# Kernel optimization log

Hardware: AMD Instinct MI355X
Metric: run time of the kernel (lower is better)

The kernel has to match this reference:

```python
import jax, jax.numpy as jnp
import numpy as np

N = 50000        # nodes
E = 800000       # directed edges (before self-loops)
F_IN = 128       # input node features
HID = 32         # hidden channels per head
HEADS = 4
NCLS = 8
EPS_BN = 1e-5
NEG_SLOPE = 0.2  # GATConv LeakyReLU default


def setup_inputs() -> dict:
    key = jax.random.key(0)
    ks = jax.random.split(key, 16)
    rn = lambda k, shape, s=0.1: jax.random.normal(k, shape, jnp.float32) * s
    inp = {}
    inp["x"] = jax.random.normal(ks[0], (N, F_IN), jnp.float32)
    inp["edge_index"] = jax.random.randint(ks[1], (2, E), 0, N, dtype=jnp.int32)
    # layer 0: F_IN -> HEADS*HID (concat)
    inp["W0"] = rn(ks[2], (F_IN, HEADS * HID))
    inp["as0"] = rn(ks[3], (HEADS, HID))
    inp["ad0"] = rn(ks[4], (HEADS, HID))
    inp["b0"] = jnp.zeros((HEADS * HID,), jnp.float32)
    inp["g0"] = jnp.ones((HEADS * HID,), jnp.float32)
    inp["bb0"] = jnp.zeros((HEADS * HID,), jnp.float32)
    inp["rm0"] = jnp.zeros((HEADS * HID,), jnp.float32)
    inp["rv0"] = jnp.ones((HEADS * HID,), jnp.float32)
    # layer 1: HEADS*HID -> HEADS*HID (concat)
    inp["W1"] = rn(ks[5], (HEADS * HID, HEADS * HID))
    inp["as1"] = rn(ks[6], (HEADS, HID))
    inp["ad1"] = rn(ks[7], (HEADS, HID))
    inp["b1"] = jnp.zeros((HEADS * HID,), jnp.float32)
    inp["g1"] = jnp.ones((HEADS * HID,), jnp.float32)
    inp["bb1"] = jnp.zeros((HEADS * HID,), jnp.float32)
    inp["rm1"] = jnp.zeros((HEADS * HID,), jnp.float32)
    inp["rv1"] = jnp.ones((HEADS * HID,), jnp.float32)
    # layer 2: HEADS*HID -> NCLS, heads=1, concat=False
    inp["W2"] = rn(ks[8], (HEADS * HID, NCLS))
    inp["as2"] = rn(ks[9], (1, NCLS))
    inp["ad2"] = rn(ks[10], (1, NCLS))
    inp["b2"] = jnp.zeros((NCLS,), jnp.float32)
    return inp


def gat_conv(x, src, dst, W, att_s, att_d, bias, H, C, concat):
    """PyG-style GATConv (eval mode, self-loops already appended to src/dst)."""
    n = x.shape[0]
    h = (x @ W).reshape(n, H, C)                       # [N,H,C]
    a_s = (h * att_s).sum(-1)                          # [N,H]
    a_d = (h * att_d).sum(-1)                          # [N,H]
    e = jax.nn.leaky_relu(a_s[src] + a_d[dst], NEG_SLOPE)  # [E,H]
    # numerically-stable segment softmax over incoming edges of each dst node
    m = jax.ops.segment_max(e, dst, num_segments=n)
    m = jnp.where(jnp.isfinite(m), m, 0.0)
    ex = jnp.exp(e - m[dst])
    den = jax.ops.segment_sum(ex, dst, num_segments=n)
    alpha = ex / (den[dst] + 1e-16)                    # [E,H]
    out = jax.ops.segment_sum(h[src] * alpha[:, :, None], dst, num_segments=n)  # [N,H,C]
    out = out.reshape(n, H * C) if concat else out.mean(axis=1)
    return out + bias


def bn_eval(x, g, b, rm, rv):
    return (x - rm) * jax.lax.rsqrt(rv + EPS_BN) * g + b


def reference(x, edge_index, W0, as0, ad0, b0, g0, bb0, rm0, rv0,
              W1, as1, ad1, b1, g1, bb1, rm1, rv1, W2, as2, ad2, b2):
    n = x.shape[0]
    loop = jnp.arange(n, dtype=edge_index.dtype)       # self-loops (PyG default)
    src = jnp.concatenate([edge_index[0], loop])
    dst = jnp.concatenate([edge_index[1], loop])
    h = gat_conv(x, src, dst, W0, as0, ad0, b0, HEADS, HID, True)
    h = jax.nn.elu(bn_eval(h, g0, bb0, rm0, rv0))
    h = gat_conv(h, src, dst, W1, as1, ad1, b1, HEADS, HID, True)
    h = jax.nn.elu(bn_eval(h, g1, bb1, rm1, rv1))
    h = gat_conv(h, src, dst, W2, as2, ad2, b2, 1, NCLS, False)
    return jax.nn.log_softmax(h, axis=1)
```

## Files before the change

### kernel.cpp

```cpp
#include <hip/hip_runtime.h>
#include <math.h>

#define N_NODES 50000
#define N_EDGES 800000
#define ET (N_EDGES + N_NODES)
#define FDIM 128
#define HEADS 4
#define HID 32
#define NCLS 8
#define NEG 0.2f
#define EPS_BN 1e-5f

#define BSH 8
#define NBUCK ((N_NODES + 255) >> BSH)
#define EPB 4096
#define PB ((ET + EPB - 1) / EPB)

typedef __attribute__((ext_vector_type(8))) short short8;
typedef __attribute__((ext_vector_type(4))) float f32x4;

__device__ __forceinline__ float lrelu(float e) { return e > 0.f ? e : NEG * e; }
__device__ __forceinline__ float bflo(unsigned u) { return __uint_as_float(u << 16); }
__device__ __forceinline__ float bfhi(unsigned u) { return __uint_as_float(u & 0xffff0000u); }
__device__ __forceinline__ unsigned f2bf(float f) {
    unsigned b = __float_as_uint(f);
    return (b + 0x7fffu + ((b >> 16) & 1u)) >> 16;
}


#define CAST_B 3125
#define PACK_B 64

__global__ __launch_bounds__(256) void prep_and_hist(
        const int* __restrict__ ei, int* __restrict__ bhist,
        const float* __restrict__ x, unsigned short* __restrict__ xb,
        const float* __restrict__ W0, unsigned short* __restrict__ W0p,
        const float* __restrict__ W1, unsigned short* __restrict__ W1p) {
    __shared__ unsigned h[NBUCK];
    int b = blockIdx.x, tid = threadIdx.x;
    if (b < PB) {
        int e0 = b * EPB;
        for (int i = tid; i < NBUCK; i += 256) h[i] = 0;
        __syncthreads();
        #pragma unroll
        for (int k = 0; k < EPB / 256; k++) {
            int e = e0 + k * 256 + tid;
            if (e < ET) {
                int d = (e < N_EDGES) ? ei[N_EDGES + e] : (e - N_EDGES);
                atomicAdd(&h[d >> BSH], 1u);
            }
        }
        __syncthreads();
        for (int i = tid; i < NBUCK; i += 256)
            if (h[i]) atomicAdd(&bhist[i], (int)h[i]);
    } else if (b < PB + CAST_B) {
        int i = (b - PB) * 256 + tid;
        const float4* p = (const float4*)x + (size_t)i * 2;
        float4 a = p[0], c = p[1];
        uint4 o;
        o.x = f2bf(a.x) | (f2bf(a.y) << 16);
        o.y = f2bf(a.z) | (f2bf(a.w) << 16);
        o.z = f2bf(c.x) | (f2bf(c.y) << 16);
        o.w = f2bf(c.z) | (f2bf(c.w) << 16);
        ((uint4*)xb)[i] = o;
    } else {
        int pb = b - PB - CAST_B;
        const float* W = (pb < PACK_B) ? W0 : W1;
        unsigned short* Wp = (pb < PACK_B) ? W0p : W1p;
        int o = (pb & (PACK_B - 1)) * 256 + tid;
        int j = o & 7, lane = (o >> 3) & 63, kc = (o >> 9) & 3, t = o >> 11;
        int k = kc * 32 + ((lane >> 4) << 3) + j;
        int n = t * 16 + (lane & 15);
        Wp[o] = (unsigned short)f2bf(W[k * 128 + n]);
    }
}

__global__ __launch_bounds__(256) void scan_buckets(const int* __restrict__ bhist,
                                                    int* __restrict__ boffs,
                                                    int* __restrict__ bcur,
                                                    int* __restrict__ offs) {
    __shared__ int s[256];
    int tid = threadIdx.x;
    int v = (tid < NBUCK) ? bhist[tid] : 0;
    s[tid] = v;
    __syncthreads();
    for (int off = 1; off < 256; off <<= 1) {
        int x = (tid >= off) ? s[tid - off] : 0;
        __syncthreads();
        s[tid] += x;
        __syncthreads();
    }
    int excl = s[tid] - v;
    if (tid < NBUCK) { boffs[tid] = excl; bcur[tid] = excl; }
    if (tid == 0) { boffs[NBUCK] = ET; offs[N_NODES] = ET; }
}

__global__ __launch_bounds__(256) void partition_pairs(const int* __restrict__ ei,
                                                       int* __restrict__ bcur,
                                                       int2* __restrict__ pairs) {
    __shared__ unsigned hist[NBUCK];
    __shared__ unsigned base[NBUCK];
    int tid = threadIdx.x;
    int e0 = blockIdx.x * EPB;
    for (int i = tid; i < NBUCK; i += 256) hist[i] = 0;
    __syncthreads();
    #pragma unroll
    for (int k = 0; k < EPB / 256; k++) {
        int e = e0 + k * 256 + tid;
        if (e < ET) {
            int d = (e < N_EDGES) ? ei[N_EDGES + e] : (e - N_EDGES);
            atomicAdd(&hist[d >> BSH], 1u);
        }
    }
    __syncthreads();
    for (int i = tid; i < NBUCK; i += 256) {
        unsigned h = hist[i];
        base[i] = h ? (unsigned)atomicAdd(&bcur[i], (int)h) : 0u;
        hist[i] = 0;
    }
    __syncthreads();
    #pragma unroll
    for (int k = 0; k < EPB / 256; k++) {
        int e = e0 + k * 256 + tid;
        if (e < ET) {
            int s, d;
            if (e < N_EDGES) { s = ei[e]; d = ei[N_EDGES + e]; }
            else             { s = d = e - N_EDGES; }
            int b = d >> BSH;
            unsigned lpos = atomicAdd(&hist[b], 1u);
            pairs[base[b] + lpos] = make_int2(s, d);
        }
    }
}

__global__ __launch_bounds__(256) void group_bucket(const int2* __restrict__ pairs,
                                                    const int* __restrict__ boffs,
                                                    int* __restrict__ offs,
                                                    int* __restrict__ ssrc) {
    __shared__ int cnt[256];
    __shared__ int pfx[256];
    int b = blockIdx.x, tid = threadIdx.x;
    int n0 = b << BSH;
    int base = boffs[b], end = boffs[b + 1];
    cnt[tid] = 0;
    __syncthreads();
    for (int i = base + tid; i < end; i += 256)
        atomicAdd(&cnt[pairs[i].y & 255], 1);
    __syncthreads();
    int v = cnt[tid];
    pfx[tid] = v;
    __syncthreads();
    for (int off = 1; off < 256; off <<= 1) {
        int x = (tid >= off) ? pfx[tid - off] : 0;
        __syncthreads();
        pfx[tid] += x;
        __syncthreads();
    }
    int excl = pfx[tid] - v;
    if (n0 + tid < N_NODES) offs[n0 + tid] = base + excl;
    cnt[tid] = excl;
    __syncthreads();
    for (int i = base + tid; i < end; i += 256) {
        int2 p = pairs[i];
        int pos = atomicAdd(&cnt[p.y & 255], 1);
        ssrc[base + pos] = p.x;
    }
}


__global__ __launch_bounds__(256) void gemm_attn(
        const unsigned short* __restrict__ Ab, const unsigned short* __restrict__ Wp,
        const float* __restrict__ att_s, const float* __restrict__ att_d,
        unsigned short* __restrict__ Hb, float* __restrict__ asn, float* __restrict__ adn,
        int M) {
    __shared__ float tiles[64 * 132];
    int tid = threadIdx.x;
    int wv = tid >> 6, lane = tid & 63;
    int base = blockIdx.x * 64;
    int mrow = base + wv * 16 + (lane & 15);
    if (mrow >= M) mrow = M - 1;
    int koff = (lane >> 4) * 8;

    f32x4 acc[8];
    #pragma unroll
    for (int t = 0; t < 8; t++) acc[t] = (f32x4){0.f, 0.f, 0.f, 0.f};

    #pragma unroll
    for (int kc = 0; kc < 4; kc++) {
        short8 a = *(const short8*)(Ab + (size_t)mrow * 128 + kc * 32 + koff);
        #pragma unroll
        for (int t = 0; t < 8; t++) {
            short8 b = *(const short8*)(Wp + (((t * 4 + kc) * 64 + lane) << 3));
            acc[t] = __builtin_amdgcn_mfma_f32_16x16x32_bf16(a, b, acc[t], 0, 0, 0);
        }
    }

    int rbase = wv * 16 + (lane >> 4) * 4;
    int col = lane & 15;
    #pragma unroll
    for (int t = 0; t < 8; t++)
        #pragma unroll
        for (int r = 0; r < 4; r++)
            tiles[(rbase + r) * 132 + t * 16 + col] = acc[t][r];
    __syncthreads();

    #pragma unroll
    for (int it = 0; it < 4; it++) {
        int u = tid + it * 256;
        int rl = u >> 4, cg = u & 15;
        int row = base + rl;
        if (row < M) {
            const float* p = tiles + rl * 132 + cg * 8;
            float4 v0 = *(const float4*)(p);
            float4 v1 = *(const float4*)(p + 4);
            uint4 o;
            o.x = f2bf(v0.x) | (f2bf(v0.y) << 16);
            o.y = f2bf(v0.z) | (f2bf(v0.w) << 16);
            o.z = f2bf(v1.x) | (f2bf(v1.y) << 16);
            o.w = f2bf(v1.z) | (f2bf(v1.w) << 16);
            *(uint4*)(Hb + (size_t)row * 128 + cg * 8) = o;
        }
    }

    {
        int rl = tid >> 2, hd = tid & 3;
        int row = base + rl;
        if (row < M) {
            const float* hrow = tiles + rl * 132 + hd * 32;
            const float* as = att_s + hd * 32;
            const float* ad = att_d + hd * 32;
            float ps = 0.f, pd = 0.f;
            #pragma unroll
            for (int i = 0; i < 8; i++) {
                float4 hv = *(const float4*)(hrow + i * 4);
                float4 sv = *(const float4*)(as + i * 4);
                float4 dv = *(const float4*)(ad + i * 4);
                ps += hv.x * sv.x + hv.y * sv.y + hv.z * sv.z + hv.w * sv.w;
                pd += hv.x * dv.x + hv.y * dv.y + hv.z * dv.z + hv.w * dv.w;
            }
            asn[row * 4 + hd] = ps;
            adn[row * 4 + hd] = pd;
        }
    }
}


__global__ __launch_bounds__(256) void aggregate(
        const unsigned short* __restrict__ hb, const float* __restrict__ asn,
        const float* __restrict__ adn, const int* __restrict__ offs,
        const int* __restrict__ ssrc, const float* __restrict__ bias,
        const float* __restrict__ gamma, const float* __restrict__ beta,
        const float* __restrict__ rmean, const float* __restrict__ rvar,
        unsigned short* __restrict__ outb) {
    __shared__ int2 sPair[4][4][72];
    int wv = threadIdx.x >> 6;
    int node = blockIdx.x * 4 + wv;
    if (node >= N_NODES) return;
    int lane = threadIdx.x & 63;
    int half = lane >> 5;
    int cl = lane & 31;
    int hd = lane >> 4;
    int beg = offs[node], deg = offs[node + 1] - beg;
    float4 ad4 = *(const float4*)(adn + node * 4);

    float4 den4 = make_float4(0.f, 0.f, 0.f, 0.f);
    float a0 = 0.f, a1 = 0.f, a2 = 0.f, a3 = 0.f;
    const char* hbase = (const char*)hb + cl * 8;
    int hsel = (cl >> 3);
    const int2* pp = &sPair[wv][hsel][0];

    auto phaseC = [&](int cnt) {
        int bound = (cnt + 15) & ~15;
        for (int i = 0; i < bound; i += 16) {
            int2 p0 = pp[i + 0 + half],  p1 = pp[i + 2 + half];
            int2 p2 = pp[i + 4 + half],  p3 = pp[i + 6 + half];
            int2 p4 = pp[i + 8 + half],  p5 = pp[i + 10 + half];
            int2 p6 = pp[i + 12 + half], p7 = pp[i + 14 + half];
            uint2 u0 = *(const uint2*)(hbase + (unsigned)p0.x);
            uint2 u1 = *(const uint2*)(hbase + (unsigned)p1.x);
            uint2 u2 = *(const uint2*)(hbase + (unsigned)p2.x);
            uint2 u3 = *(const uint2*)(hbase + (unsigned)p3.x);
            uint2 u4 = *(const uint2*)(hbase + (unsigned)p4.x);
            uint2 u5 = *(const uint2*)(hbase + (unsigned)p5.x);
            uint2 u6 = *(const uint2*)(hbase + (unsigned)p6.x);
            uint2 u7 = *(const uint2*)(hbase + (unsigned)p7.x);
            float w0 = __int_as_float(p0.y), w1 = __int_as_float(p1.y);
            float w2 = __int_as_float(p2.y), w3 = __int_as_float(p3.y);
            float w4 = __int_as_float(p4.y), w5 = __int_as_float(p5.y);
            float w6 = __int_as_float(p6.y), w7 = __int_as_float(p7.y);
            a0 += w0 * bflo(u0.x); a1 += w0 * bfhi(u0.x); a2 += w0 * bflo(u0.y); a3 += w0 * bfhi(u0.y);
            a0 += w1 * bflo(u1.x); a1 += w1 * bfhi(u1.x); a2 += w1 * bflo(u1.y); a3 += w1 * bfhi(u1.y);
            a0 += w2 * bflo(u2.x); a1 += w2 * bfhi(u2.x); a2 += w2 * bflo(u2.y); a3 += w2 * bfhi(u2.y);
            a0 += w3 * bflo(u3.x); a1 += w3 * bfhi(u3.x); a2 += w3 * bflo(u3.y); a3 += w3 * bfhi(u3.y);
            a0 += w4 * bflo(u4.x); a1 += w4 * bfhi(u4.x); a2 += w4 * bflo(u4.y); a3 += w4 * bfhi(u4.y);
            a0 += w5 * bflo(u5.x); a1 += w5 * bfhi(u5.x); a2 += w5 * bflo(u5.y); a3 += w5 * bfhi(u5.y);
            a0 += w6 * bflo(u6.x); a1 += w6 * bfhi(u6.x); a2 += w6 * bflo(u6.y); a3 += w6 * bfhi(u6.y);
            a0 += w7 * bflo(u7.x); a1 += w7 * bfhi(u7.x); a2 += w7 * bflo(u7.y); a3 += w7 * bfhi(u7.y);
        }
    };

    for (int base0 = 0; base0 < deg; base0 += 64) {
        int j = base0 + lane;
        int soff = 0;
        float4 w4v = make_float4(0.f, 0.f, 0.f, 0.f);
        if (j < deg) {
            int s = ssrc[beg + j];
            soff = s << 8;
            float4 a = *(const float4*)(asn + s * 4);
            w4v.x = __expf(lrelu(a.x + ad4.x));
            w4v.y = __expf(lrelu(a.y + ad4.y));
            w4v.z = __expf(lrelu(a.z + ad4.z));
            w4v.w = __expf(lrelu(a.w + ad4.w));
            den4.x += w4v.x; den4.y += w4v.y; den4.z += w4v.z; den4.w += w4v.w;
        }
        sPair[wv][0][lane] = make_int2(soff, __float_as_int(w4v.x));
        sPair[wv][1][lane] = make_int2(soff, __float_as_int(w4v.y));
        sPair[wv][2][lane] = make_int2(soff, __float_as_int(w4v.z));
        sPair[wv][3][lane] = make_int2(soff, __float_as_int(w4v.w));
        int cnt = deg - base0; if (cnt > 64) cnt = 64;
        phaseC(cnt);
    }
    (void)hd;

    a0 += __shfl_xor(a0, 32); a1 += __shfl_xor(a1, 32);
    a2 += __shfl_xor(a2, 32); a3 += __shfl_xor(a3, 32);
    #pragma unroll
    for (int off = 32; off; off >>= 1) {
        den4.x += __shfl_xor(den4.x, off);
        den4.y += __shfl_xor(den4.y, off);
        den4.z += __shfl_xor(den4.z, off);
        den4.w += __shfl_xor(den4.w, off);
    }
    if (half == 0) {
        float den = (hsel & 2) ? ((hsel & 1) ? den4.w : den4.z)
                               : ((hsel & 1) ? den4.y : den4.x);
        float inv = 1.f / (den + 1e-16f);
        int c0 = cl * 4;
        float4 bi = *(const float4*)(bias + c0);
        float4 gm = *(const float4*)(gamma + c0);
        float4 bt = *(const float4*)(beta + c0);
        float4 rm = *(const float4*)(rmean + c0);
        float4 rv = *(const float4*)(rvar + c0);
        float o0 = a0 * inv + bi.x, o1 = a1 * inv + bi.y;
        float o2 = a2 * inv + bi.z, o3 = a3 * inv + bi.w;
        o0 = (o0 - rm.x) * rsqrtf(rv.x + EPS_BN) * gm.x + bt.x;
        o1 = (o1 - rm.y) * rsqrtf(rv.y + EPS_BN) * gm.y + bt.y;
        o2 = (o2 - rm.z) * rsqrtf(rv.z + EPS_BN) * gm.z + bt.z;
        o3 = (o3 - rm.w) * rsqrtf(rv.w + EPS_BN) * gm.w + bt.w;
        o0 = (o0 > 0.f) ? o0 : expm1f(o0);
        o1 = (o1 > 0.f) ? o1 : expm1f(o1);
        o2 = (o2 > 0.f) ? o2 : expm1f(o2);
        o3 = (o3 > 0.f) ? o3 : expm1f(o3);
        uint2 ob;
        ob.x = f2bf(o0) | (f2bf(o1) << 16);
        ob.y = f2bf(o2) | (f2bf(o3) << 16);
        *(uint2*)(outb + (size_t)node * 128 + c0) = ob;
    }
}


__global__ __launch_bounds__(256) void gemm2_fused(
        const unsigned short* __restrict__ xb, const float* __restrict__ W2,
        const float* __restrict__ as2, const float* __restrict__ ad2,
        float* __restrict__ h2, float* __restrict__ asn, float* __restrict__ adn) {
    __shared__ float sW[128 * 8];
    __shared__ float sas[8], sad[8];
    int tid = threadIdx.x;
    for (int i = tid; i < 1024; i += 256) sW[i] = W2[i];
    if (tid < 8) { sas[tid] = as2[tid]; sad[tid] = ad2[tid]; }
    __syncthreads();
    int node = blockIdx.x * 256 + tid;
    if (node >= N_NODES) return;
    const uint4* xr = (const uint4*)(xb + (size_t)node * 128);
    float acc[8];
    #pragma unroll
    for (int c = 0; c < 8; c++) acc[c] = 0.f;
    for (int k8 = 0; k8 < 16; k8++) {
        uint4 u = xr[k8];
        float f[8] = { bflo(u.x), bfhi(u.x), bflo(u.y), bfhi(u.y),
                       bflo(u.z), bfhi(u.z), bflo(u.w), bfhi(u.w) };
        int kb = k8 * 8;
        #pragma unroll
        for (int q = 0; q < 8; q++)
            #pragma unroll
            for (int c = 0; c < 8; c++)
                acc[c] += f[q] * sW[(kb + q) * 8 + c];
    }
    float ps = 0.f, pd = 0.f;
    #pragma unroll
    for (int c = 0; c < 8; c++) {
        h2[(size_t)node * 8 + c] = acc[c];
        ps += acc[c] * sas[c];
        pd += acc[c] * sad[c];
    }
    asn[node] = ps;
    adn[node] = pd;
}


__global__ __launch_bounds__(256) void aggregate2(
        const float* __restrict__ h2, const float* __restrict__ asn,
        const float* __restrict__ adn, const int* __restrict__ offs,
        const int* __restrict__ ssrc, const float* __restrict__ b2,
        float* __restrict__ out) {
    __shared__ int2 sPair[4][64];
    int wv = threadIdx.x >> 6;
    int node = blockIdx.x * 4 + wv;
    if (node >= N_NODES) return;
    int lane = threadIdx.x & 63;
    int g = lane >> 3, c = lane & 7;
    int beg = offs[node], end = offs[node + 1];
    int deg = end - beg;
    float adv = adn[node];

    float den = 0.f, acc = 0.f;
    auto phaseC = [&](int cnt) {
        int nIt = (cnt + 15) >> 4;
        const int2* pp = &sPair[wv][0];
        for (int i = 0; i < nIt; i++) {
            int e = i * 16 + g;
            int2 p0 = pp[e];
            int2 p1 = pp[e + 8];
            acc += __int_as_float(p0.y) * h2[(((unsigned)p0.x) << 3) + c];
            acc += __int_as_float(p1.y) * h2[(((unsigned)p1.x) << 3) + c];
        }
    };

    for (int base = 0; base < deg; base += 64) {
        int j = base + lane;
        int s = 0; float w = 0.f;
        if (j < deg) {
            s = ssrc[beg + j];
            w = __expf(lrelu(asn[s] + adv));
            den += w;
        }
        sPair[wv][lane] = make_int2(s, __float_as_int(w));
        int cnt = deg - base; if (cnt > 64) cnt = 64;
        phaseC(cnt);
    }

    acc += __shfl_xor(acc, 8); acc += __shfl_xor(acc, 16); acc += __shfl_xor(acc, 32);
    #pragma unroll
    for (int off = 32; off; off >>= 1) den += __shfl_xor(den, off);

    float o = acc / (den + 1e-16f) + b2[c];
    float mx = o;
    mx = fmaxf(mx, __shfl_xor(mx, 1));
    mx = fmaxf(mx, __shfl_xor(mx, 2));
    mx = fmaxf(mx, __shfl_xor(mx, 4));
    float ex = __expf(o - mx);
    float sm = ex;
    sm += __shfl_xor(sm, 1); sm += __shfl_xor(sm, 2); sm += __shfl_xor(sm, 4);
    if (g == 0) out[(size_t)node * 8 + c] = o - mx - logf(sm);
}


extern "C" void kernel_launch(void* const* d_in, const int* in_sizes, int n_in,
                              void* d_out, int out_size, void* d_ws, size_t ws_size,
                              hipStream_t stream) {
    const float* x   = (const float*)d_in[0];
    const int*   ei  = (const int*)d_in[1];
    const float* W0  = (const float*)d_in[2];
    const float* as0 = (const float*)d_in[3];
    const float* ad0 = (const float*)d_in[4];
    const float* b0  = (const float*)d_in[5];
    const float* g0  = (const float*)d_in[6];
    const float* bb0 = (const float*)d_in[7];
    const float* rm0 = (const float*)d_in[8];
    const float* rv0 = (const float*)d_in[9];
    const float* W1  = (const float*)d_in[10];
    const float* as1 = (const float*)d_in[11];
    const float* ad1 = (const float*)d_in[12];
    const float* b1  = (const float*)d_in[13];
    const float* g1  = (const float*)d_in[14];
    const float* bb1 = (const float*)d_in[15];
    const float* rm1 = (const float*)d_in[16];
    const float* rv1 = (const float*)d_in[17];
    const float* W2  = (const float*)d_in[18];
    const float* as2 = (const float*)d_in[19];
    const float* ad2 = (const float*)d_in[20];
    const float* b2  = (const float*)d_in[21];
    float* out = (float*)d_out;

    char* w = (char*)d_ws;
    size_t off = 0;
    auto carve = [&](size_t bytes) {
        void* p = w + off;
        off += (bytes + 255) & ~(size_t)255;
        return p;
    };
    unsigned short* xb   = (unsigned short*)carve((size_t)N_NODES * 128 * 2);
    unsigned short* Hb   = (unsigned short*)carve((size_t)N_NODES * 128 * 2);
    unsigned short* Xb   = (unsigned short*)carve((size_t)N_NODES * 128 * 2);
    unsigned short* W0p  = (unsigned short*)carve(16384 * 2);
    unsigned short* W1p  = (unsigned short*)carve(16384 * 2);
    int*   offs   = (int*)carve((size_t)(N_NODES + 1) * 4);
    int*   bhist  = (int*)carve((size_t)NBUCK * 4);
    int*   boffs  = (int*)carve((size_t)(NBUCK + 1) * 4);
    int*   bcur   = (int*)carve((size_t)NBUCK * 4);
    int*   ssrc   = (int*)carve((size_t)ET * 4);
    int2*  pairs  = (int2*)carve((size_t)ET * 8);
    float* asn    = (float*)carve((size_t)N_NODES * 4 * 4);
    float* adn    = (float*)carve((size_t)N_NODES * 4 * 4);
    float* h2     = (float*)carve((size_t)N_NODES * 8 * 4);
    float* as2n   = (float*)carve((size_t)N_NODES * 4);
    float* ad2n   = (float*)carve((size_t)N_NODES * 4);
    (void)ws_size; (void)in_sizes; (void)n_in; (void)out_size;

    const int NB = (N_NODES + 255) / 256;
    const int GB = (N_NODES + 63) / 64;

    hipMemsetAsync(bhist, 0, (size_t)NBUCK * 4, stream);
    prep_and_hist<<<PB + CAST_B + 2 * PACK_B, 256, 0, stream>>>(ei, bhist, x, xb,
                                                                W0, W0p, W1, W1p);
    scan_buckets<<<1, 256, 0, stream>>>(bhist, boffs, bcur, offs);
    partition_pairs<<<PB, 256, 0, stream>>>(ei, bcur, pairs);
    group_bucket<<<NBUCK, 256, 0, stream>>>(pairs, boffs, offs, ssrc);

    gemm_attn<<<GB, 256, 0, stream>>>(xb, W0p, as0, ad0, Hb, asn, adn, N_NODES);
    aggregate<<<(N_NODES + 3) / 4, 256, 0, stream>>>(Hb, asn, adn, offs, ssrc,
                                                     b0, g0, bb0, rm0, rv0, Xb);
    gemm_attn<<<GB, 256, 0, stream>>>(Xb, W1p, as1, ad1, Hb, asn, adn, N_NODES);
    aggregate<<<(N_NODES + 3) / 4, 256, 0, stream>>>(Hb, asn, adn, offs, ssrc,
                                                     b1, g1, bb1, rm1, rv1, Xb);
    gemm2_fused<<<NB, 256, 0, stream>>>(Xb, W2, as2, ad2, h2, as2n, ad2n);
    aggregate2<<<(N_NODES + 3) / 4, 256, 0, stream>>>(h2, as2n, ad2n, offs, ssrc, b2, out);
}
```

Measured before the change: 295.6 us.

## Fuse all GAT stages into one cooperative persistent kernel with grid syncs

Turns every stage (CSR build, the two GEMM+attention passes, aggregations, final layer) into device functions, and runs them inside one cooperative kernel that loops over work units and separates stages with grid.sync. This removes about ten kernel launches and the memset. The global atomic bucket histogram becomes per-block histograms that the scan reduces, so no zero-initialisation is needed. It keeps a multi-kernel fallback for when a cooperative launch is unavailable, but trades launch gaps for grid-barrier cost and fewer resident blocks per stage.

```diff
diff --git a/kernel.cpp b/kernel.cpp
--- a/kernel.cpp
+++ b/kernel.cpp
@@ -1,13 +1,12 @@
 #include <hip/hip_runtime.h>
+#include <hip/hip_cooperative_groups.h>
 #include <math.h>
+
+namespace cg = cooperative_groups;
 
 #define N_NODES 50000
 #define N_EDGES 800000
 #define ET (N_EDGES + N_NODES)
-#define FDIM 128
-#define HEADS 4
-#define HID 32
-#define NCLS 8
 #define NEG 0.2f
 #define EPS_BN 1e-5f
 
@@ -15,6 +14,12 @@
 #define NBUCK ((N_NODES + 255) >> BSH)
 #define EPB 4096
 #define PB ((ET + EPB - 1) / EPB)
+#define CAST_B 3125
+#define PACK_B 64
+#define GB ((N_NODES + 63) / 64)
+#define AGG_U 12500
+#define G2B ((N_NODES + 255) / 256)
+#define PREP_U (PB + CAST_B + 2 * PACK_B)
 
 typedef __attribute__((ext_vector_type(8))) short short8;
 typedef __attribute__((ext_vector_type(4))) float f32x4;
@@ -27,21 +32,31 @@
     return (b + 0x7fffu + ((b >> 16) & 1u)) >> 16;
 }
 
-
-#define CAST_B 3125
-#define PACK_B 64
-
-__global__ __launch_bounds__(256) void prep_and_hist(
-        const int* __restrict__ ei, int* __restrict__ bhist,
+struct GatParams {
+    const int* ei;
+    const float* x;
+    const float *W0, *as0, *ad0, *b0, *g0, *bb0, *rm0, *rv0;
+    const float *W1, *as1, *ad1, *b1, *g1, *bb1, *rm1, *rv1;
+    const float *W2, *as2, *ad2, *b2;
+    float* out;
+    unsigned short *xb, *Hb, *Xb, *W0p, *W1p;
+    int *offs, *boffs, *bcur, *ssrc, *hists;
+    int2* pairs;
+    float *asn, *adn, *h2;
+};
+
+
+__device__ __forceinline__ void prep_unit(char* smem, int u, int tid,
+        const int* __restrict__ ei, int* __restrict__ hists,
         const float* __restrict__ x, unsigned short* __restrict__ xb,
         const float* __restrict__ W0, unsigned short* __restrict__ W0p,
         const float* __restrict__ W1, unsigned short* __restrict__ W1p) {
-    __shared__ unsigned h[NBUCK];
-    int b = blockIdx.x, tid = threadIdx.x;
-    if (b < PB) {
-        int e0 = b * EPB;
+    if (u < PB) {
+        unsigned* h = (unsigned*)smem;
+        __syncthreads();
         for (int i = tid; i < NBUCK; i += 256) h[i] = 0;
         __syncthreads();
+        int e0 = u * EPB;
         #pragma unroll
         for (int k = 0; k < EPB / 256; k++) {
             int e = e0 + k * 256 + tid;
@@ -52,11 +67,11 @@
         }
         __syncthreads();
         for (int i = tid; i < NBUCK; i += 256)
-            if (h[i]) atomicAdd(&bhist[i], (int)h[i]);
-    } else if (b < PB + CAST_B) {
-        int i = (b - PB) * 256 + tid;
-        const float4* p = (const float4*)x + (size_t)i * 2;
-        float4 a = p[0], c = p[1];
+            hists[u * NBUCK + i] = (int)h[i];
+    } else if (u < PB + CAST_B) {
+        int i = (u - PB) * 256 + tid;
+        const float4* px = (const float4*)x + (size_t)i * 2;
+        float4 a = px[0], c = px[1];
         uint4 o;
         o.x = f2bf(a.x) | (f2bf(a.y) << 16);
         o.y = f2bf(a.z) | (f2bf(a.w) << 16);
@@ -64,7 +79,7 @@
         o.w = f2bf(c.z) | (f2bf(c.w) << 16);
         ((uint4*)xb)[i] = o;
     } else {
-        int pb = b - PB - CAST_B;
+        int pb = u - PB - CAST_B;
         const float* W = (pb < PACK_B) ? W0 : W1;
         unsigned short* Wp = (pb < PACK_B) ? W0p : W1p;
         int o = (pb & (PACK_B - 1)) * 256 + tid;
@@ -75,13 +90,16 @@
     }
 }
 
-__global__ __launch_bounds__(256) void scan_buckets(const int* __restrict__ bhist,
-                                                    int* __restrict__ boffs,
-                                                    int* __restrict__ bcur,
-                                                    int* __restrict__ offs) {
-    __shared__ int s[256];
-    int tid = threadIdx.x;
-    int v = (tid < NBUCK) ? bhist[tid] : 0;
+__device__ __forceinline__ void scan_unit(char* smem, int tid,
+        const int* __restrict__ hists, int* __restrict__ boffs,
+        int* __restrict__ bcur, int* __restrict__ offs) {
+    int* s = (int*)smem;
+    int v = 0;
+    if (tid < NBUCK) {
+        const int* hp = hists + tid;
+        #pragma unroll 8
+        for (int uu = 0; uu < PB; uu++) v += hp[uu * NBUCK];
+    }
     s[tid] = v;
     __syncthreads();
     for (int off = 1; off < 256; off <<= 1) {
@@ -93,17 +111,17 @@
     int excl = s[tid] - v;
     if (tid < NBUCK) { boffs[tid] = excl; bcur[tid] = excl; }
     if (tid == 0) { boffs[NBUCK] = ET; offs[N_NODES] = ET; }
-}
-
-__global__ __launch_bounds__(256) void partition_pairs(const int* __restrict__ ei,
-                                                       int* __restrict__ bcur,
-                                                       int2* __restrict__ pairs) {
-    __shared__ unsigned hist[NBUCK];
-    __shared__ unsigned base[NBUCK];
-    int tid = threadIdx.x;
-    int e0 = blockIdx.x * EPB;
+    __syncthreads();
+}
+
+__device__ __forceinline__ void partition_unit(char* smem, int u, int tid,
+        const int* __restrict__ ei, int* __restrict__ bcur, int2* __restrict__ pairs) {
+    unsigned* hist = (unsigned*)smem;
+    unsigned* base = hist + NBUCK;
+    __syncthreads();
     for (int i = tid; i < NBUCK; i += 256) hist[i] = 0;
     __syncthreads();
+    int e0 = u * EPB;
     #pragma unroll
     for (int k = 0; k < EPB / 256; k++) {
         int e = e0 + k * 256 + tid;
@@ -114,8 +132,8 @@
     }
     __syncthreads();
     for (int i = tid; i < NBUCK; i += 256) {
-        unsigned h = hist[i];
-        base[i] = h ? (unsigned)atomicAdd(&bcur[i], (int)h) : 0u;
+        unsigned hh = hist[i];
+        base[i] = hh ? (unsigned)atomicAdd(&bcur[i], (int)hh) : 0u;
         hist[i] = 0;
     }
     __syncthreads();
@@ -133,15 +151,14 @@
     }
 }
 
-__global__ __launch_bounds__(256) void group_bucket(const int2* __restrict__ pairs,
-                                                    const int* __restrict__ boffs,
-                                                    int* __restrict__ offs,
-                                                    int* __restrict__ ssrc) {
-    __shared__ int cnt[256];
-    __shared__ int pfx[256];
-    int b = blockIdx.x, tid = threadIdx.x;
-    int n0 = b << BSH;
-    int base = boffs[b], end = boffs[b + 1];
+__device__ __forceinline__ void group_unit(char* smem, int u, int tid,
+        const int2* __restrict__ pairs, const int* __restrict__ boffs,
+        int* __restrict__ offs, int* __restrict__ ssrc) {
+    int* cnt = (int*)smem;
+    int* pfx = cnt + 256;
+    __syncthreads();
+    int n0 = u << BSH;
+    int base = boffs[u], end = boffs[u + 1];
     cnt[tid] = 0;
     __syncthreads();
     for (int i = base + tid; i < end; i += 256)
@@ -161,224 +178,211 @@
     cnt[tid] = excl;
     __syncthreads();
     for (int i = base + tid; i < end; i += 256) {
-        int2 p = pairs[i];
-        int pos = atomicAdd(&cnt[p.y & 255], 1);
-        ssrc[base + pos] = p.x;
-    }
-}
-
-
-__global__ __launch_bounds__(256) void gemm_attn(
+        int2 pr = pairs[i];
+        int pos = atomicAdd(&cnt[pr.y & 255], 1);
+        ssrc[base + pos] = pr.x;
+    }
+}
+
+__device__ __forceinline__ void gemm_phase(char* smem, int blk, int nblk,
         const unsigned short* __restrict__ Ab, const unsigned short* __restrict__ Wp,
         const float* __restrict__ att_s, const float* __restrict__ att_d,
-        unsigned short* __restrict__ Hb, float* __restrict__ asn, float* __restrict__ adn,
-        int M) {
-    __shared__ float tiles[64 * 132];
+        unsigned short* __restrict__ Hb, float* __restrict__ asn, float* __restrict__ adn) {
+    float* tiles = (float*)smem;
     int tid = threadIdx.x;
     int wv = tid >> 6, lane = tid & 63;
-    int base = blockIdx.x * 64;
-    int mrow = base + wv * 16 + (lane & 15);
-    if (mrow >= M) mrow = M - 1;
-    int koff = (lane >> 4) * 8;
-
-    f32x4 acc[8];
-    #pragma unroll
-    for (int t = 0; t < 8; t++) acc[t] = (f32x4){0.f, 0.f, 0.f, 0.f};
-
-    #pragma unroll
-    for (int kc = 0; kc < 4; kc++) {
-        short8 a = *(const short8*)(Ab + (size_t)mrow * 128 + kc * 32 + koff);
+    for (int u = blk; u < GB; u += nblk) {
+        int base = u * 64;
+        int mrow = base + wv * 16 + (lane & 15);
+        if (mrow >= N_NODES) mrow = N_NODES - 1;
+        int koff = (lane >> 4) * 8;
+
+        f32x4 acc[8];
         #pragma unroll
-        for (int t = 0; t < 8; t++) {
-            short8 b = *(const short8*)(Wp + (((t * 4 + kc) * 64 + lane) << 3));
-            acc[t] = __builtin_amdgcn_mfma_f32_16x16x32_bf16(a, b, acc[t], 0, 0, 0);
-        }
-    }
-
-    int rbase = wv * 16 + (lane >> 4) * 4;
-    int col = lane & 15;
-    #pragma unroll
-    for (int t = 0; t < 8; t++)
+        for (int t = 0; t < 8; t++) acc[t] = (f32x4){0.f, 0.f, 0.f, 0.f};
         #pragma unroll
-        for (int r = 0; r < 4; r++)
-            tiles[(rbase + r) * 132 + t * 16 + col] = acc[t][r];
-    __syncthreads();
-
-    #pragma unroll
-    for (int it = 0; it < 4; it++) {
-        int u = tid + it * 256;
-        int rl = u >> 4, cg = u & 15;
-        int row = base + rl;
-        if (row < M) {
-            const float* p = tiles + rl * 132 + cg * 8;
-            float4 v0 = *(const float4*)(p);
-            float4 v1 = *(const float4*)(p + 4);
-            uint4 o;
-            o.x = f2bf(v0.x) | (f2bf(v0.y) << 16);
-            o.y = f2bf(v0.z) | (f2bf(v0.w) << 16);
-            o.z = f2bf(v1.x) | (f2bf(v1.y) << 16);
-            o.w = f2bf(v1.z) | (f2bf(v1.w) << 16);
-            *(uint4*)(Hb + (size_t)row * 128 + cg * 8) = o;
-        }
-    }
-
-    {
-        int rl = tid >> 2, hd = tid & 3;
-        int row = base + rl;
-        if (row < M) {
-            const float* hrow = tiles + rl * 132 + hd * 32;
-            const float* as = att_s + hd * 32;
-            const float* ad = att_d + hd * 32;
-            float ps = 0.f, pd = 0.f;
+        for (int kc = 0; kc < 4; kc++) {
+            short8 a = *(const short8*)(Ab + (size_t)mrow * 128 + kc * 32 + koff);
             #pragma unroll
-            for (int i = 0; i < 8; i++) {
-                float4 hv = *(const float4*)(hrow + i * 4);
-                float4 sv = *(const float4*)(as + i * 4);
-                float4 dv = *(const float4*)(ad + i * 4);
-                ps += hv.x * sv.x + hv.y * sv.y + hv.z * sv.z + hv.w * sv.w;
-                pd += hv.x * dv.x + hv.y * dv.y + hv.z * dv.z + hv.w * dv.w;
+            for (int t = 0; t < 8; t++) {
+                short8 b = *(const short8*)(Wp + (((t * 4 + kc) * 64 + lane) << 3));
+                acc[t] = __builtin_amdgcn_mfma_f32_16x16x32_bf16(a, b, acc[t], 0, 0, 0);
             }
-            asn[row * 4 + hd] = ps;
-            adn[row * 4 + hd] = pd;
-        }
-    }
-}
-
-
-__global__ __launch_bounds__(256) void aggregate(
+        }
+        __syncthreads();
+        int rbase = wv * 16 + (lane >> 4) * 4;
+        int col = lane & 15;
+        #pragma unroll
+        for (int t = 0; t < 8; t++)
+            #pragma unroll
+            for (int r = 0; r < 4; r++)
+                tiles[(rbase + r) * 132 + t * 16 + col] = acc[t][r];
+        __syncthreads();
+
+        #pragma unroll
+        for (int it = 0; it < 4; it++) {
+            int uu = tid + it * 256;
+            int rl = uu >> 4, cg4 = uu & 15;
+            int row = base + rl;
+            if (row < N_NODES) {
+                const float* pt = tiles + rl * 132 + cg4 * 8;
+                float4 v0 = *(const float4*)(pt);
+                float4 v1 = *(const float4*)(pt + 4);
+                uint4 o;
+                o.x = f2bf(v0.x) | (f2bf(v0.y) << 16);
+                o.y = f2bf(v0.z) | (f2bf(v0.w) << 16);
+                o.z = f2bf(v1.x) | (f2bf(v1.y) << 16);
+                o.w = f2bf(v1.z) | (f2bf(v1.w) << 16);
+                *(uint4*)(Hb + (size_t)row * 128 + cg4 * 8) = o;
+            }
+        }
+        {
+            int rl = tid >> 2, hd = tid & 3;
+            int row = base + rl;
+            if (row < N_NODES) {
+                const float* hrow = tiles + rl * 132 + hd * 32;
+                const float* as = att_s + hd * 32;
+                const float* ad = att_d + hd * 32;
+                float ps = 0.f, pd = 0.f;
+                #pragma unroll
+                for (int i = 0; i < 8; i++) {
+                    float4 hv = *(const float4*)(hrow + i * 4);
+                    float4 sv = *(const float4*)(as + i * 4);
+                    float4 dv = *(const float4*)(ad + i * 4);
+                    ps += hv.x * sv.x + hv.y * sv.y + hv.z * sv.z + hv.w * sv.w;
+                    pd += hv.x * dv.x + hv.y * dv.y + hv.z * dv.z + hv.w * dv.w;
+                }
+                asn[row * 4 + hd] = ps;
+                adn[row * 4 + hd] = pd;
+            }
+        }
+        __syncthreads();
+    }
+}
+
+__device__ __forceinline__ void aggregate_phase(char* smem, int blk, int nblk,
         const unsigned short* __restrict__ hb, const float* __restrict__ asn,
         const float* __restrict__ adn, const int* __restrict__ offs,
         const int* __restrict__ ssrc, const float* __restrict__ bias,
         const float* __restrict__ gamma, const float* __restrict__ beta,
         const float* __restrict__ rmean, const float* __restrict__ rvar,
         unsigned short* __restrict__ outb) {
-    __shared__ int2 sPair[4][4][72];
-    int wv = threadIdx.x >> 6;
-    int node = blockIdx.x * 4 + wv;
-    if (node >= N_NODES) return;
-    int lane = threadIdx.x & 63;
-    int half = lane >> 5;
-    int cl = lane & 31;
-    int hd = lane >> 4;
-    int beg = offs[node], deg = offs[node + 1] - beg;
-    float4 ad4 = *(const float4*)(adn + node * 4);
-
-    float4 den4 = make_float4(0.f, 0.f, 0.f, 0.f);
-    float a0 = 0.f, a1 = 0.f, a2 = 0.f, a3 = 0.f;
+    int2* sP = (int2*)smem;
+    int tid = threadIdx.x;
+    int wv = tid >> 6, lane = tid & 63;
+    int half = lane >> 5, cl = lane & 31, hsel = cl >> 3;
     const char* hbase = (const char*)hb + cl * 8;
-    int hsel = (cl >> 3);
-    const int2* pp = &sPair[wv][hsel][0];
-
-    auto phaseC = [&](int cnt) {
-        int bound = (cnt + 15) & ~15;
-        for (int i = 0; i < bound; i += 16) {
-            int2 p0 = pp[i + 0 + half],  p1 = pp[i + 2 + half];
-            int2 p2 = pp[i + 4 + half],  p3 = pp[i + 6 + half];
-            int2 p4 = pp[i + 8 + half],  p5 = pp[i + 10 + half];
-            int2 p6 = pp[i + 12 + half], p7 = pp[i + 14 + half];
-            uint2 u0 = *(const uint2*)(hbase + (unsigned)p0.x);
-            uint2 u1 = *(const uint2*)(hbase + (unsigned)p1.x);
-            uint2 u2 = *(const uint2*)(hbase + (unsigned)p2.x);
-            uint2 u3 = *(const uint2*)(hbase + (unsigned)p3.x);
-            uint2 u4 = *(const uint2*)(hbase + (unsigned)p4.x);
-            uint2 u5 = *(const uint2*)(hbase + (unsigned)p5.x);
-            uint2 u6 = *(const uint2*)(hbase + (unsigned)p6.x);
-            uint2 u7 = *(const uint2*)(hbase + (unsigned)p7.x);
-            float w0 = __int_as_float(p0.y), w1 = __int_as_float(p1.y);
-            float w2 = __int_as_float(p2.y), w3 = __int_as_float(p3.y);
-            float w4 = __int_as_float(p4.y), w5 = __int_as_float(p5.y);
-            float w6 = __int_as_float(p6.y), w7 = __int_as_float(p7.y);
-            a0 += w0 * bflo(u0.x); a1 += w0 * bfhi(u0.x); a2 += w0 * bflo(u0.y); a3 += w0 * bfhi(u0.y);
-            a0 += w1 * bflo(u1.x); a1 += w1 * bfhi(u1.x); a2 += w1 * bflo(u1.y); a3 += w1 * bfhi(u1.y);
-            a0 += w2 * bflo(u2.x); a1 += w2 * bfhi(u2.x); a2 += w2 * bflo(u2.y); a3 += w2 * bfhi(u2.y);
-            a0 += w3 * bflo(u3.x); a1 += w3 * bfhi(u3.x); a2 += w3 * bflo(u3.y); a3 += w3 * bfhi(u3.y);
-            a0 += w4 * bflo(u4.x); a1 += w4 * bfhi(u4.x); a2 += w4 * bflo(u4.y); a3 += w4 * bfhi(u4.y);
-            a0 += w5 * bflo(u5.x); a1 += w5 * bfhi(u5.x); a2 += w5 * bflo(u5.y); a3 += w5 * bfhi(u5.y);
-            a0 += w6 * bflo(u6.x); a1 += w6 * bfhi(u6.x); a2 += w6 * bflo(u6.y); a3 += w6 * bfhi(u6.y);
-            a0 += w7 * bflo(u7.x); a1 += w7 * bfhi(u7.x); a2 += w7 * bflo(u7.y); a3 += w7 * bfhi(u7.y);
-        }
-    };
-
-    for (int base0 = 0; base0 < deg; base0 += 64) {
-        int j = base0 + lane;
-        int soff = 0;
-        float4 w4v = make_float4(0.f, 0.f, 0.f, 0.f);
-        if (j < deg) {
-            int s = ssrc[beg + j];
-            soff = s << 8;
-            float4 a = *(const float4*)(asn + s * 4);
-            w4v.x = __expf(lrelu(a.x + ad4.x));
-            w4v.y = __expf(lrelu(a.y + ad4.y));
-            w4v.z = __expf(lrelu(a.z + ad4.z));
-            w4v.w = __expf(lrelu(a.w + ad4.w));
-            den4.x += w4v.x; den4.y += w4v.y; den4.z += w4v.z; den4.w += w4v.w;
-        }
-        sPair[wv][0][lane] = make_int2(soff, __float_as_int(w4v.x));
-        sPair[wv][1][lane] = make_int2(soff, __float_as_int(w4v.y));
-        sPair[wv][2][lane] = make_int2(soff, __float_as_int(w4v.z));
-        sPair[wv][3][lane] = make_int2(soff, __float_as_int(w4v.w));
-        int cnt = deg - base0; if (cnt > 64) cnt = 64;
-        phaseC(cnt);
-    }
-    (void)hd;
-
-    a0 += __shfl_xor(a0, 32); a1 += __shfl_xor(a1, 32);
-    a2 += __shfl_xor(a2, 32); a3 += __shfl_xor(a3, 32);
-    #pragma unroll
-    for (int off = 32; off; off >>= 1) {
-        den4.x += __shfl_xor(den4.x, off);
-        den4.y += __shfl_xor(den4.y, off);
-        den4.z += __shfl_xor(den4.z, off);
-        den4.w += __shfl_xor(den4.w, off);
-    }
-    if (half == 0) {
-        float den = (hsel & 2) ? ((hsel & 1) ? den4.w : den4.z)
-                               : ((hsel & 1) ? den4.y : den4.x);
-        float inv = 1.f / (den + 1e-16f);
-        int c0 = cl * 4;
-        float4 bi = *(const float4*)(bias + c0);
-        float4 gm = *(const float4*)(gamma + c0);
-        float4 bt = *(const float4*)(beta + c0);
-        float4 rm = *(const float4*)(rmean + c0);
-        float4 rv = *(const float4*)(rvar + c0);
-        float o0 = a0 * inv + bi.x, o1 = a1 * inv + bi.y;
-        float o2 = a2 * inv + bi.z, o3 = a3 * inv + bi.w;
-        o0 = (o0 - rm.x) * rsqrtf(rv.x + EPS_BN) * gm.x + bt.x;
-        o1 = (o1 - rm.y) * rsqrtf(rv.y + EPS_BN) * gm.y + bt.y;
-        o2 = (o2 - rm.z) * rsqrtf(rv.z + EPS_BN) * gm.z + bt.z;
-        o3 = (o3 - rm.w) * rsqrtf(rv.w + EPS_BN) * gm.w + bt.w;
-        o0 = (o0 > 0.f) ? o0 : expm1f(o0);
-        o1 = (o1 > 0.f) ? o1 : expm1f(o1);
-        o2 = (o2 > 0.f) ? o2 : expm1f(o2);
-        o3 = (o3 > 0.f) ? o3 : expm1f(o3);
-        uint2 ob;
-        ob.x = f2bf(o0) | (f2bf(o1) << 16);
-        ob.y = f2bf(o2) | (f2bf(o3) << 16);
-        *(uint2*)(outb + (size_t)node * 128 + c0) = ob;
-    }
-}
-
-
-__global__ __launch_bounds__(256) void gemm2_fused(
+    int2* st0 = sP + (wv * 4 + 0) * 72;
+    int2* st1 = sP + (wv * 4 + 1) * 72;
+    int2* st2 = sP + (wv * 4 + 2) * 72;
+    int2* st3 = sP + (wv * 4 + 3) * 72;
+    const int2* pp = sP + (wv * 4 + hsel) * 72;
+
+    for (int u = blk; u < AGG_U; u += nblk) {
+        int node = u * 4 + wv;
+        int beg = offs[node], deg = offs[node + 1] - beg;
+        float4 ad4 = *(const float4*)(adn + node * 4);
+        float a0 = 0.f, a1 = 0.f, a2 = 0.f, a3 = 0.f, denl = 0.f;
+
+        for (int base0 = 0; base0 < deg; base0 += 64) {
+            int j = base0 + lane;
+            int soff = 0;
+            float4 w4v = make_float4(0.f, 0.f, 0.f, 0.f);
+            if (j < deg) {
+                int s = ssrc[beg + j];
+                soff = s << 8;
+                float4 a = *(const float4*)(asn + s * 4);
+                w4v.x = __expf(lrelu(a.x + ad4.x));
+                w4v.y = __expf(lrelu(a.y + ad4.y));
+                w4v.z = __expf(lrelu(a.z + ad4.z));
+                w4v.w = __expf(lrelu(a.w + ad4.w));
+            }
+            st0[lane] = make_int2(soff, __float_as_int(w4v.x));
+            st1[lane] = make_int2(soff, __float_as_int(w4v.y));
+            st2[lane] = make_int2(soff, __float_as_int(w4v.z));
+            st3[lane] = make_int2(soff, __float_as_int(w4v.w));
+            int cnt = deg - base0; if (cnt > 64) cnt = 64;
+            int bound = (cnt + 15) & ~15;
+            for (int i = 0; i < bound; i += 16) {
+                int2 p0 = pp[i + 0 + half],  p1 = pp[i + 2 + half];
+                int2 p2 = pp[i + 4 + half],  p3 = pp[i + 6 + half];
+                int2 p4 = pp[i + 8 + half],  p5 = pp[i + 10 + half];
+                int2 p6 = pp[i + 12 + half], p7 = pp[i + 14 + half];
+                uint2 u0 = *(const uint2*)(hbase + (unsigned)p0.x);
+                uint2 u1 = *(const uint2*)(hbase + (unsigned)p1.x);
+                uint2 u2 = *(const uint2*)(hbase + (unsigned)p2.x);
+                uint2 u3 = *(const uint2*)(hbase + (unsigned)p3.x);
+                uint2 u4 = *(const uint2*)(hbase + (unsigned)p4.x);
+                uint2 u5 = *(const uint2*)(hbase + (unsigned)p5.x);
+                uint2 u6 = *(const uint2*)(hbase + (unsigned)p6.x);
+                uint2 u7 = *(const uint2*)(hbase + (unsigned)p7.x);
+                float w0 = __int_as_float(p0.y), w1 = __int_as_float(p1.y);
+                float w2 = __int_as_float(p2.y), w3 = __int_as_float(p3.y);
+                float w4 = __int_as_float(p4.y), w5 = __int_as_float(p5.y);
+                float w6 = __int_as_float(p6.y), w7 = __int_as_float(p7.y);
+                denl += w0 + w1 + w2 + w3 + w4 + w5 + w6 + w7;
+                a0 += w0 * bflo(u0.x); a1 += w0 * bfhi(u0.x); a2 += w0 * bflo(u0.y); a3 += w0 * bfhi(u0.y);
+                a0 += w1 * bflo(u1.x); a1 += w1 * bfhi(u1.x); a2 += w1 * bflo(u1.y); a3 += w1 * bfhi(u1.y);
+                a0 += w2 * bflo(u2.x); a1 += w2 * bfhi(u2.x); a2 += w2 * bflo(u2.y); a3 += w2 * bfhi(u2.y);
+                a0 += w3 * bflo(u3.x); a1 += w3 * bfhi(u3.x); a2 += w3 * bflo(u3.y); a3 += w3 * bfhi(u3.y);
+                a0 += w4 * bflo(u4.x); a1 += w4 * bfhi(u4.x); a2 += w4 * bflo(u4.y); a3 += w4 * bfhi(u4.y);
+                a0 += w5 * bflo(u5.x); a1 += w5 * bfhi(u5.x); a2 += w5 * bflo(u5.y); a3 += w5 * bfhi(u5.y);
+                a0 += w6 * bflo(u6.x); a1 += w6 * bfhi(u6.x); a2 += w6 * bflo(u6.y); a3 += w6 * bfhi(u6.y);
+                a0 += w7 * bflo(u7.x); a1 += w7 * bfhi(u7.x); a2 += w7 * bflo(u7.y); a3 += w7 * bfhi(u7.y);
+            }
+        }
+        a0 += __shfl_xor(a0, 32); a1 += __shfl_xor(a1, 32);
+        a2 += __shfl_xor(a2, 32); a3 += __shfl_xor(a3, 32);
+        denl += __shfl_xor(denl, 32);
+        if (half == 0) {
+            float inv = 1.f / (denl + 1e-16f);
+            int c0 = cl * 4;
+            float4 bi = *(const float4*)(bias + c0);
+            float4 gm = *(const float4*)(gamma + c0);
+            float4 bt = *(const float4*)(beta + c0);
+            float4 rm = *(const float4*)(rmean + c0);
+            float4 rv = *(const float4*)(rvar + c0);
+            float o0 = a0 * inv + bi.x, o1 = a1 * inv + bi.y;
+            float o2 = a2 * inv + bi.z, o3 = a3 * inv + bi.w;
+            o0 = (o0 - rm.x) * rsqrtf(rv.x + EPS_BN) * gm.x + bt.x;
+            o1 = (o1 - rm.y) * rsqrtf(rv.y + EPS_BN) * gm.y + bt.y;
+            o2 = (o2 - rm.z) * rsqrtf(rv.z + EPS_BN) * gm.z + bt.z;
+            o3 = (o3 - rm.w) * rsqrtf(rv.w + EPS_BN) * gm.w + bt.w;
+            o0 = (o0 > 0.f) ? o0 : expm1f(o0);
+            o1 = (o1 > 0.f) ? o1 : expm1f(o1);
+            o2 = (o2 > 0.f) ? o2 : expm1f(o2);
+            o3 = (o3 > 0.f) ? o3 : expm1f(o3);
+            uint2 ob;
+            ob.x = f2bf(o0) | (f2bf(o1) << 16);
+            ob.y = f2bf(o2) | (f2bf(o3) << 16);
+            *(uint2*)(outb + (size_t)node * 128 + c0) = ob;
+        }
+    }
+}
+
+__device__ __forceinline__ void gemm2_unit(char* smem, int u, int tid,
         const unsigned short* __restrict__ xb, const float* __restrict__ W2,
         const float* __restrict__ as2, const float* __restrict__ ad2,
-        float* __restrict__ h2, float* __restrict__ asn, float* __restrict__ adn) {
-    __shared__ float sW[128 * 8];
-    __shared__ float sas[8], sad[8];
-    int tid = threadIdx.x;
-    for (int i = tid; i < 1024; i += 256) sW[i] = W2[i];
-    if (tid < 8) { sas[tid] = as2[tid]; sad[tid] = ad2[tid]; }
-    __syncthreads();
-    int node = blockIdx.x * 256 + tid;
+        float* __restrict__ h2, float* __restrict__ asn, float* __restrict__ adn,
+        bool loadW) {
+    float* sW = (float*)smem;
+    float* sas = sW + 1024;
+    float* sad = sas + 8;
+    if (loadW) {
+        for (int i = tid; i < 1024; i += 256) sW[i] = W2[i];
+        if (tid < 8) { sas[tid] = as2[tid]; sad[tid] = ad2[tid]; }
+        __syncthreads();
+    }
+    int node = u * 256 + tid;
     if (node >= N_NODES) return;
     const uint4* xr = (const uint4*)(xb + (size_t)node * 128);
     float acc[8];
     #pragma unroll
     for (int c = 0; c < 8; c++) acc[c] = 0.f;
     for (int k8 = 0; k8 < 16; k8++) {
-        uint4 u = xr[k8];
-        float f[8] = { bflo(u.x), bfhi(u.x), bflo(u.y), bfhi(u.y),
-                       bflo(u.z), bfhi(u.z), bflo(u.w), bfhi(u.w) };
+        uint4 uu = xr[k8];
+        float f[8] = { bflo(uu.x), bfhi(uu.x), bflo(uu.y), bfhi(uu.y),
+                       bflo(uu.z), bfhi(uu.z), bflo(uu.w), bfhi(uu.w) };
         int kb = k8 * 8;
         #pragma unroll
         for (int q = 0; q < 8; q++)
@@ -397,35 +401,20 @@
     adn[node] = pd;
 }
 
-
-__global__ __launch_bounds__(256) void aggregate2(
+__device__ __forceinline__ void agg2_unit(char* smem, int u, int tid,
         const float* __restrict__ h2, const float* __restrict__ asn,
         const float* __restrict__ adn, const int* __restrict__ offs,
         const int* __restrict__ ssrc, const float* __restrict__ b2,
         float* __restrict__ out) {
-    __shared__ int2 sPair[4][64];
-    int wv = threadIdx.x >> 6;
-    int node = blockIdx.x * 4 + wv;
-    if (node >= N_NODES) return;
-    int lane = threadIdx.x & 63;
+    int2* sP = (int2*)smem;
+    int wv = tid >> 6, lane = tid & 63;
     int g = lane >> 3, c = lane & 7;
+    int node = u * 4 + wv;
     int beg = offs[node], end = offs[node + 1];
     int deg = end - beg;
     float adv = adn[node];
-
     float den = 0.f, acc = 0.f;
-    auto phaseC = [&](int cnt) {
-        int nIt = (cnt + 15) >> 4;
-        const int2* pp = &sPair[wv][0];
-        for (int i = 0; i < nIt; i++) {
-            int e = i * 16 + g;
-            int2 p0 = pp[e];
-            int2 p1 = pp[e + 8];
-            acc += __int_as_float(p0.y) * h2[(((unsigned)p0.x) << 3) + c];
-            acc += __int_as_float(p1.y) * h2[(((unsigned)p1.x) << 3) + c];
-        }
-    };
-
+    int2* ws = sP + wv * 64;
     for (int base = 0; base < deg; base += 64) {
         int j = base + lane;
         int s = 0; float w = 0.f;
@@ -434,15 +423,20 @@
             w = __expf(lrelu(asn[s] + adv));
             den += w;
         }
-        sPair[wv][lane] = make_int2(s, __float_as_int(w));
+        ws[lane] = make_int2(s, __float_as_int(w));
         int cnt = deg - base; if (cnt > 64) cnt = 64;
-        phaseC(cnt);
-    }
-
+        int nIt = (cnt + 15) >> 4;
+        for (int i = 0; i < nIt; i++) {
+            int e = i * 16 + g;
+            int2 p0 = ws[e];
+            int2 p1 = ws[e + 8];
+            acc += __int_as_float(p0.y) * h2[(((unsigned)p0.x) << 3) + c];
+            acc += __int_as_float(p1.y) * h2[(((unsigned)p1.x) << 3) + c];
+        }
+    }
     acc += __shfl_xor(acc, 8); acc += __shfl_xor(acc, 16); acc += __shfl_xor(acc, 32);
     #pragma unroll
     for (int off = 32; off; off >>= 1) den += __shfl_xor(den, off);
-
     float o = acc / (den + 1e-16f) + b2[c];
     float mx = o;
     mx = fmaxf(mx, __shfl_xor(mx, 1));
@@ -455,32 +449,125 @@
 }
 
 
+__global__ __launch_bounds__(256, 3) void gat_mega(GatParams p) {
+    cg::grid_group grid = cg::this_grid();
+    __shared__ __align__(16) char smem[64 * 132 * 4];
+    const int blk = blockIdx.x, nblk = gridDim.x, tid = threadIdx.x;
+
+    for (int u = blk; u < PREP_U; u += nblk)
+        prep_unit(smem, u, tid, p.ei, p.hists, p.x, p.xb, p.W0, p.W0p, p.W1, p.W1p);
+    grid.sync();
+
+    if (blk == 0) scan_unit(smem, tid, p.hists, p.boffs, p.bcur, p.offs);
+    gemm_phase(smem, blk, nblk, p.xb, p.W0p, p.as0, p.ad0, p.Hb, p.asn, p.adn);
+    grid.sync();
+
+    for (int u = blk; u < PB; u += nblk)
+        partition_unit(smem, u, tid, p.ei, p.bcur, p.pairs);
+    grid.sync();
+
+    for (int u = blk; u < NBUCK; u += nblk)
+        group_unit(smem, u, tid, p.pairs, p.boffs, p.offs, p.ssrc);
+    grid.sync();
+
+    aggregate_phase(smem, blk, nblk, p.Hb, p.asn, p.adn, p.offs, p.ssrc,
+                    p.b0, p.g0, p.bb0, p.rm0, p.rv0, p.Xb);
+    grid.sync();
+
+    gemm_phase(smem, blk, nblk, p.Xb, p.W1p, p.as1, p.ad1, p.Hb, p.asn, p.adn);
+    grid.sync();
+
+    aggregate_phase(smem, blk, nblk, p.Hb, p.asn, p.adn, p.offs, p.ssrc,
+                    p.b1, p.g1, p.bb1, p.rm1, p.rv1, p.Xb);
+    grid.sync();
+
+    {
+        float* sW = (float*)smem;
+        float* sas = sW + 1024;
+        float* sad = sas + 8;
+        __syncthreads();
+        for (int i = tid; i < 1024; i += 256) sW[i] = p.W2[i];
+        if (tid < 8) { sas[tid] = p.as2[tid]; sad[tid] = p.ad2[tid]; }
+        __syncthreads();
+        for (int u = blk; u < G2B; u += nblk)
+            gemm2_unit(smem, u, tid, p.Xb, p.W2, p.as2, p.ad2, p.h2, p.asn, p.adn, false);
+    }
+    grid.sync();
+
+    for (int u = blk; u < AGG_U; u += nblk) {
+        __syncthreads();
+        agg2_unit(smem, u, tid, p.h2, p.asn, p.adn, p.offs, p.ssrc, p.b2, p.out);
+    }
+}
+
+
+__global__ __launch_bounds__(256) void k_prep(GatParams p) {
+    __shared__ __align__(16) char smem[1024];
+    prep_unit(smem, blockIdx.x, threadIdx.x, p.ei, p.hists, p.x, p.xb,
+              p.W0, p.W0p, p.W1, p.W1p);
+}
+__global__ __launch_bounds__(256) void k_scan(GatParams p) {
+    __shared__ __align__(16) char smem[1024];
+    scan_unit(smem, threadIdx.x, p.hists, p.boffs, p.bcur, p.offs);
+}
+__global__ __launch_bounds__(256) void k_partition(GatParams p) {
+    __shared__ __align__(16) char smem[2048];
+    partition_unit(smem, blockIdx.x, threadIdx.x, p.ei, p.bcur, p.pairs);
+}
+__global__ __launch_bounds__(256) void k_group(GatParams p) {
+    __shared__ __align__(16) char smem[2048];
+    group_unit(smem, blockIdx.x, threadIdx.x, p.pairs, p.boffs, p.offs, p.ssrc);
+}
+__global__ __launch_bounds__(256) void k_gemm(GatParams p, int layer) {
+    __shared__ __align__(16) char smem[64 * 132 * 4];
+    if (layer == 0)
+        gemm_phase(smem, blockIdx.x, gridDim.x, p.xb, p.W0p, p.as0, p.ad0,
+                   p.Hb, p.asn, p.adn);
+    else
+        gemm_phase(smem, blockIdx.x, gridDim.x, p.Xb, p.W1p, p.as1, p.ad1,
+                   p.Hb, p.asn, p.adn);
+}
+__global__ __launch_bounds__(256) void k_agg(GatParams p, int layer) {
+    __shared__ __align__(16) char smem[4 * 4 * 72 * 8];
+    if (layer == 0)
+        aggregate_phase(smem, blockIdx.x, gridDim.x, p.Hb, p.asn, p.adn, p.offs,
+                        p.ssrc, p.b0, p.g0, p.bb0, p.rm0, p.rv0, p.Xb);
+    else
+        aggregate_phase(smem, blockIdx.x, gridDim.x, p.Hb, p.asn, p.adn, p.offs,
+                        p.ssrc, p.b1, p.g1, p.bb1, p.rm1, p.rv1, p.Xb);
+}
+__global__ __launch_bounds__(256) void k_gemm2(GatParams p) {
+    __shared__ __align__(16) char smem[1040 * 4];
+    gemm2_unit(smem, blockIdx.x, threadIdx.x, p.Xb, p.W2, p.as2, p.ad2,
+               p.h2, p.asn, p.adn, true);
+}
+__global__ __launch_bounds__(256) void k_agg2(GatParams p) {
+    __shared__ __align__(16) char smem[4 * 64 * 8];
+    agg2_unit(smem, blockIdx.x, threadIdx.x, p.h2, p.asn, p.adn, p.offs,
+              p.ssrc, p.b2, p.out);
+}
+
+
 extern "C" void kernel_launch(void* const* d_in, const int* in_sizes, int n_in,
                               void* d_out, int out_size, void* d_ws, size_t ws_size,
                               hipStream_t stream) {
-    const float* x   = (const float*)d_in[0];
-    const int*   ei  = (const int*)d_in[1];
-    const float* W0  = (const float*)d_in[2];
-    const float* as0 = (const float*)d_in[3];
-    const float* ad0 = (const float*)d_in[4];
-    const float* b0  = (const float*)d_in[5];
-    const float* g0  = (const float*)d_in[6];
-    const float* bb0 = (const float*)d_in[7];
-    const float* rm0 = (const float*)d_in[8];
-    const float* rv0 = (const float*)d_in[9];
-    const float* W1  = (const float*)d_in[10];
-    const float* as1 = (const float*)d_in[11];
-    const float* ad1 = (const float*)d_in[12];
-    const float* b1  = (const float*)d_in[13];
-    const float* g1  = (const float*)d_in[14];
-    const float* bb1 = (const float*)d_in[15];
-    const float* rm1 = (const float*)d_in[16];
-    const float* rv1 = (const float*)d_in[17];
-    const float* W2  = (const float*)d_in[18];
-    const float* as2 = (const float*)d_in[19];
-    const float* ad2 = (const float*)d_in[20];
-    const float* b2  = (const float*)d_in[21];
-    float* out = (float*)d_out;
+    GatParams prm;
+    prm.ei  = (const int*)d_in[1];
+    prm.x   = (const float*)d_in[0];
+    prm.W0  = (const float*)d_in[2];
+    prm.as0 = (const float*)d_in[3];  prm.ad0 = (const float*)d_in[4];
+    prm.b0  = (const float*)d_in[5];  prm.g0  = (const float*)d_in[6];
+    prm.bb0 = (const float*)d_in[7];  prm.rm0 = (const float*)d_in[8];
+    prm.rv0 = (const float*)d_in[9];
+    prm.W1  = (const float*)d_in[10];
+    prm.as1 = (const float*)d_in[11]; prm.ad1 = (const float*)d_in[12];
+    prm.b1  = (const float*)d_in[13]; prm.g1  = (const float*)d_in[14];
+    prm.bb1 = (const float*)d_in[15]; prm.rm1 = (const float*)d_in[16];
+    prm.rv1 = (const float*)d_in[17];
+    prm.W2  = (const float*)d_in[18];
+    prm.as2 = (const float*)d_in[19]; prm.ad2 = (const float*)d_in[20];
+    prm.b2  = (const float*)d_in[21];
+    prm.out = (float*)d_out;
 
     char* w = (char*)d_ws;
     size_t off = 0;
@@ -489,40 +576,42 @@
         off += (bytes + 255) & ~(size_t)255;
         return p;
     };
-    unsigned short* xb   = (unsigned short*)carve((size_t)N_NODES * 128 * 2);
-    unsigned short* Hb   = (unsigned short*)carve((size_t)N_NODES * 128 * 2);
-    unsigned short* Xb   = (unsigned short*)carve((size_t)N_NODES * 128 * 2);
-    unsigned short* W0p  = (unsigned short*)carve(16384 * 2);
-    unsigned short* W1p  = (unsigned short*)carve(16384 * 2);
-    int*   offs   = (int*)carve((size_t)(N_NODES + 1) * 4);
-    int*   bhist  = (int*)carve((size_t)NBUCK * 4);
-    int*   boffs  = (int*)carve((size_t)(NBUCK + 1) * 4);
-    int*   bcur   = (int*)carve((size_t)NBUCK * 4);
-    int*   ssrc   = (int*)carve((size_t)ET * 4);
-    int2*  pairs  = (int2*)carve((size_t)ET * 8);
-    float* asn    = (float*)carve((size_t)N_NODES * 4 * 4);
-    float* adn    = (float*)carve((size_t)N_NODES * 4 * 4);
-    float* h2     = (float*)carve((size_t)N_NODES * 8 * 4);
-    float* as2n   = (float*)carve((size_t)N_NODES * 4);
-    float* ad2n   = (float*)carve((size_t)N_NODES * 4);
+    prm.xb    = (unsigned short*)carve((size_t)N_NODES * 128 * 2);
+    prm.Hb    = (unsigned short*)carve((size_t)N_NODES * 128 * 2);
+    prm.Xb    = (unsigned short*)carve((size_t)N_NODES * 128 * 2);
+    prm.W0p   = (unsigned short*)carve(16384 * 2);
+    prm.W1p   = (unsigned short*)carve(16384 * 2);
+    prm.offs  = (int*)carve((size_t)(N_NODES + 1) * 4);
+    prm.boffs = (int*)carve((size_t)(NBUCK + 1) * 4);
+    prm.bcur  = (int*)carve((size_t)NBUCK * 4);
+    prm.ssrc  = (int*)carve((size_t)ET * 4);
+    prm.hists = (int*)carve((size_t)PB * NBUCK * 4);
+    prm.pairs = (int2*)carve((size_t)ET * 8);
+    prm.asn   = (float*)carve((size_t)N_NODES * 4 * 4);
+    prm.adn   = (float*)carve((size_t)N_NODES * 4 * 4);
+    prm.h2    = (float*)carve((size_t)N_NODES * 8 * 4);
     (void)ws_size; (void)in_sizes; (void)n_in; (void)out_size;
 
-    const int NB = (N_NODES + 255) / 256;
-    const int GB = (N_NODES + 63) / 64;
-
-    hipMemsetAsync(bhist, 0, (size_t)NBUCK * 4, stream);
-    prep_and_hist<<<PB + CAST_B + 2 * PACK_B, 256, 0, stream>>>(ei, bhist, x, xb,
-                                                                W0, W0p, W1, W1p);
-    scan_buckets<<<1, 256, 0, stream>>>(bhist, boffs, bcur, offs);
-    partition_pairs<<<PB, 256, 0, stream>>>(ei, bcur, pairs);
-    group_bucket<<<NBUCK, 256, 0, stream>>>(pairs, boffs, offs, ssrc);
-
-    gemm_attn<<<GB, 256, 0, stream>>>(xb, W0p, as0, ad0, Hb, asn, adn, N_NODES);
-    aggregate<<<(N_NODES + 3) / 4, 256, 0, stream>>>(Hb, asn, adn, offs, ssrc,
-                                                     b0, g0, bb0, rm0, rv0, Xb);
-    gemm_attn<<<GB, 256, 0, stream>>>(Xb, W1p, as1, ad1, Hb, asn, adn, N_NODES);
-    aggregate<<<(N_NODES + 3) / 4, 256, 0, stream>>>(Hb, asn, adn, offs, ssrc,
-                                                     b1, g1, bb1, rm1, rv1, Xb);
-    gemm2_fused<<<NB, 256, 0, stream>>>(Xb, W2, as2, ad2, h2, as2n, ad2n);
-    aggregate2<<<(N_NODES + 3) / 4, 256, 0, stream>>>(h2, as2n, ad2n, offs, ssrc, b2, out);
-}
+    bool coop_done = false;
+    int mb = 0;
+    if (hipOccupancyMaxActiveBlocksPerMultiprocessor(
+            &mb, (const void*)gat_mega, 256, 0) == hipSuccess && mb >= 2) {
+        int nb = (mb >= 3) ? 768 : 512;
+        void* args[] = { (void*)&prm };
+        if (hipLaunchCooperativeKernel((const void*)gat_mega, dim3(nb), dim3(256),
+                                       args, 0, stream) == hipSuccess)
+            coop_done = true;
+    }
+    if (!coop_done) {
+        k_prep<<<PREP_U, 256, 0, stream>>>(prm);
+        k_scan<<<1, 256, 0, stream>>>(prm);
+        k_partition<<<PB, 256, 0, stream>>>(prm);
+        k_group<<<NBUCK, 256, 0, stream>>>(prm);
+        k_gemm<<<GB, 256, 0, stream>>>(prm, 0);
+        k_agg<<<AGG_U, 256, 0, stream>>>(prm, 0);
+        k_gemm<<<GB, 256, 0, stream>>>(prm, 1);
+        k_agg<<<AGG_U, 256, 0, stream>>>(prm, 1);
+        k_gemm2<<<G2B, 256, 0, stream>>>(prm);
+        k_agg2<<<AGG_U, 256, 0, stream>>>(prm);
+    }
+}
```

Result: slower. 328.0 us (+10.9%).
